# Kernel tuning notes

Measured on AMD Instinct MI355X. Metric: run time of the kernel, lower is better.

The kernel has to match this reference:

```python
import jax, jax.numpy as jnp
import numpy as np

N, DIM = 1024, 3
DEPTH, H1, H2, NF = 4, 64, 32, 8
L = 1.0
PI = np.pi


def _h2_features(x):
    n, dim = x.shape
    rij = x[:, None, :] - x[None, :, :]                       # (n, n, dim)
    eye = jnp.eye(n, dtype=x.dtype)
    # distance of periodic sine displacement, diagonal regularized then zeroed
    r = jnp.linalg.norm(jnp.sin(PI * rij / L) + eye[..., None], axis=-1) * (1.0 - eye)
    kf = jnp.arange(1, NF + 1, dtype=x.dtype)                 # (NF,)
    ang = (2.0 * PI / L) * rij[:, :, None, :] * kf[:, None]   # (n, n, NF, dim)
    # original concat order per frequency k: cos block (dim cols) then sin block
    cs = jnp.stack([jnp.cos(ang), jnp.sin(ang)], axis=3)      # (n, n, NF, 2, dim)
    return jnp.concatenate([r[..., None], cs.reshape(n, n, 2 * NF * dim)], axis=-1)


def _h1_init(t, n):
    t = jnp.reshape(t, ())
    kf = jnp.arange(1, NF + 1, dtype=jnp.float32)
    ang = 2.0 * PI * t * kf                                   # (NF,)
    feats = jnp.concatenate([t[None], jnp.stack([jnp.cos(ang), jnp.sin(ang)], axis=1).reshape(-1)])
    return jnp.broadcast_to(feats[None, :], (n, 1 + 2 * NF))  # (n, 17)


def _combine(h1, h2):
    n = h1.shape[0]
    g2 = jnp.mean(h2, axis=0)                                 # (n, h2f)
    g1 = jnp.broadcast_to(jnp.mean(h1, axis=0, keepdims=True), h1.shape)
    return jnp.concatenate([h1, g1, g2], axis=1)


def _forward(x, t, W1, b1, W2, b2, Wf):
    n, dim = x.shape
    h1 = _h1_init(t, n)
    h2 = _h2_features(x)
    for d in range(DEPTH - 1):
        f = _combine(h1, h2)
        h1u = jnp.tanh(f @ W1[d] + b1[d])
        h2u = jnp.tanh(h2 @ W2[d] + b2[d])
        h1 = h1u + h1 if d > 0 else h1u
        h2 = h2u + h2 if d > 0 else h2u
    f = _combine(h1, h2)
    h1 = jnp.tanh(f @ W1[-1] + b1[-1]) + h1
    force = jnp.clip(2.0 * x, -10.0, 10.0)
    return -(h1 @ Wf) * force


def setup_inputs():
    key = jax.random.key(0)
    ks = jax.random.split(key, 20)
    s = 0.01
    inp = {
        "x": jax.random.normal(ks[0], (N, DIM), jnp.float32),
        "t": jax.random.uniform(ks[1], (), dtype=jnp.float32),
    }
    f0 = 2 * (1 + 2 * NF) + (1 + 2 * NF * DIM)  # 83
    fl = 2 * H1 + H2                            # 160
    w1_in = [f0, fl, fl, fl]
    w2_in = [1 + 2 * NF * DIM, H2, H2]
    for d in range(DEPTH):
        inp[f"W1_{d}"] = s * jax.random.normal(ks[2 + d], (w1_in[d], H1), jnp.float32)
        inp[f"b1_{d}"] = jnp.zeros((H1,), jnp.float32)
    for d in range(DEPTH - 1):
        inp[f"W2_{d}"] = s * jax.random.normal(ks[8 + d], (w2_in[d], H2), jnp.float32)
        inp[f"b2_{d}"] = jnp.zeros((H2,), jnp.float32)
    inp["Wf"] = s * jax.random.normal(ks[15], (H1, DIM), jnp.float32)
    return inp


def reference(x, t, W1_0, b1_0, W1_1, b1_1, W1_2, b1_2, W1_3, b1_3,
              W2_0, b2_0, W2_1, b2_1, W2_2, b2_2, Wf):
    W1 = [W1_0, W1_1, W1_2, W1_3]
    b1 = [b1_0, b1_1, b1_2, b1_3]
    W2 = [W2_0, W2_1, W2_2]
    b2 = [b2_0, b2_1, b2_2]
    return _forward(x, t, W1, b1, W2, b2, Wf)
```

## Files before the change

### kernel.cpp

```cpp
#include <hip/hip_runtime.h>
#include <math.h>


#define NP 1024

static const size_t OF_TROW = 0;
static const size_t OF_CSUM = OF_TROW + NP*56;
static const size_t OF_SSUM = OF_CSUM + 24;
static const size_t OF_HSUM = OF_SSUM + 24;
static const size_t OF_CNT  = OF_HSUM + 192;
static const size_t OF_RACC = OF_CNT + 4;
static const size_t OF_M0   = OF_RACC + NP;
static const size_t OF_M1   = OF_M0 + NP*32;
static const size_t OF_M2   = OF_M1 + NP*32;

__device__ __forceinline__ float ftanh(float x) {
    float e = __expf(2.0f * x);
    return 1.0f - __fdividef(2.0f, e + 1.0f);
}

__global__ __launch_bounds__(1024) void k1_tables(
    const float* __restrict__ X,
    float* __restrict__ TROW,
    float* __restrict__ CSUM, float* __restrict__ SSUM,
    float* __restrict__ HSUM, int* __restrict__ CNT)
{
    const int i = threadIdx.x;
    float ck[24], sk[24], cp[3], sp[3];
#pragma unroll
    for (int d = 0; d < 3; ++d) {
        float x = X[i*3 + d];
        sincospif(x, &sp[d], &cp[d]);
#pragma unroll
        for (int k = 0; k < 8; ++k) {
            float s, c;
            sincospif(2.0f*(float)(k+1)*x, &s, &c);
            ck[k*3 + d] = c;  sk[k*3 + d] = s;
        }
    }
    float4* row = (float4*)(TROW + (size_t)i*56);
#pragma unroll
    for (int t = 0; t < 12; ++t)
        row[t] = make_float4(ck[2*t], sk[2*t], ck[2*t+1], sk[2*t+1]);
    row[12] = make_float4(cp[0], sp[0], cp[1], sp[1]);
    row[13] = make_float4(cp[2], sp[2], 0.f, 0.f);

    __shared__ float part[48*16];
    const int lane = i & 63, wv = i >> 6;
#pragma unroll
    for (int v = 0; v < 24; ++v) {
        float a = ck[v], b = sk[v];
#pragma unroll
        for (int off = 32; off; off >>= 1) {
            a += __shfl_down(a, off, 64);
            b += __shfl_down(b, off, 64);
        }
        if (lane == 0) { part[v*16 + wv] = a; part[(24+v)*16 + wv] = b; }
    }
    __syncthreads();
    if (i < 48) {
        float s = 0.f;
#pragma unroll
        for (int w = 0; w < 16; ++w) s += part[i*16 + w];
        if (i < 24) CSUM[i] = s; else SSUM[i-24] = s;
    }
    if (i < 192) HSUM[i] = 0.0f;
    if (i == 200) CNT[0] = 0;
}

__global__ __launch_bounds__(512, 4) void k2_pairs(
    const float* __restrict__ W20, const float* __restrict__ b20,
    const float* __restrict__ W21, const float* __restrict__ b21,
    const float* __restrict__ W22, const float* __restrict__ b22,
    const float* __restrict__ TROW,
    float* __restrict__ RACC, float* __restrict__ M0,
    float* __restrict__ M1, float* __restrict__ M2)
{
    __shared__ __align__(16) float sH0[128*32];
    __shared__ __align__(16) float sH1[128*32];
    __shared__ __align__(16) float sJ[56];
    __shared__ __align__(16) float sPQ[24*64];

    const int tid  = threadIdx.x;
    const int lane = tid & 63;
    const int wid  = __builtin_amdgcn_readfirstlane(tid >> 6);
    const int c0   = wid * 4;
    const int j    = blockIdx.x;
    const int lx   = lane & 7;

    if (tid < 14) ((float4*)sJ)[tid] = ((const float4*)(TROW + (size_t)j*56))[tid];

    const float b0x = b20[c0+0], b0y = b20[c0+1], b0z = b20[c0+2], b0w = b20[c0+3];
    const float b1x = b21[c0+0], b1y = b21[c0+1], b1z = b21[c0+2], b1w = b21[c0+3];
    const float b2x = b22[c0+0], b2y = b22[c0+1], b2z = b22[c0+2], b2w = b22[c0+3];
    __syncthreads();

    for (int idx = tid; idx < 24*64; idx += 512) {
        const int kd = idx >> 6;
        const int e  = idx & 63;
        const int c  = e & 31;
        const int k = kd/3, d = kd - k*3;
        const float wcv = W20[(1 + k*6 + d)*32 + c];
        const float wsv = W20[(4 + k*6 + d)*32 + c];
        const float cj = sJ[2*kd], sj = sJ[2*kd+1];
        sPQ[idx] = (e < 32) ? fmaf(cj, wcv, -(sj*wsv))
                            : fmaf(sj, wcv,   cj*wsv);
    }
    __syncthreads();

    float4* H0a = (float4*)sH0 + lane*8;
    float4* H0b = (float4*)sH0 + (lane+64)*8;
    float4* H1a = (float4*)sH1 + lane*8;
    float4* H1b = (float4*)sH1 + (lane+64)*8;

    float a0x=0.f,a0y=0.f,a0z=0.f,a0w=0.f;
    float a1x=0.f,a1y=0.f,a1z=0.f,a1w=0.f;
    float a2x=0.f,a2y=0.f,a2z=0.f,a2w=0.f;
    float racc = 0.f;

#pragma unroll 1
    for (int tile = 0; tile < 8; ++tile) {
        const float4* rowA = (const float4*)(TROW + (size_t)(tile*128 + lane)*56);
        const float4* rowB = rowA + 14*64;

        float rA, rB;
        {
            const float4 pa = rowA[12], pb = rowA[13];
            float s0 = fmaf(pa.y, sJ[48], -(pa.x * sJ[49]));
            float s1 = fmaf(pa.w, sJ[50], -(pa.z * sJ[51]));
            float s2 = fmaf(pb.y, sJ[52], -(pb.x * sJ[53]));
            rA = sqrtf(fmaf(s0, s0, fmaf(s1, s1, s2*s2)));
        }
        {
            const float4 pa = rowB[12], pb = rowB[13];
            float s0 = fmaf(pa.y, sJ[48], -(pa.x * sJ[49]));
            float s1 = fmaf(pa.w, sJ[50], -(pa.z * sJ[51]));
            float s2 = fmaf(pb.y, sJ[52], -(pb.x * sJ[53]));
            rB = sqrtf(fmaf(s0, s0, fmaf(s1, s1, s2*s2)));
        }
        racc += rA + rB;

        float zA0, zA1, zA2, zA3, zB0, zB1, zB2, zB3;
        {
            const float* w = W20 + c0;
            zA0 = fmaf(rA, w[0], b0x); zA1 = fmaf(rA, w[1], b0y);
            zA2 = fmaf(rA, w[2], b0z); zA3 = fmaf(rA, w[3], b0w);
            zB0 = fmaf(rB, w[0], b0x); zB1 = fmaf(rB, w[1], b0y);
            zB2 = fmaf(rB, w[2], b0z); zB3 = fmaf(rB, w[3], b0w);
        }
#pragma unroll
        for (int t = 0; t < 12; ++t) {
            const float4 fA = rowA[t], fB = rowB[t];
#pragma unroll
            for (int sub = 0; sub < 2; ++sub) {
                const int kd = 2*t + sub;
                const float4 P = *(const float4*)(sPQ + kd*64 + c0);
                const float4 Q = *(const float4*)(sPQ + kd*64 + 32 + c0);
                const float ciA = sub ? fA.z : fA.x, siA = sub ? fA.w : fA.y;
                const float ciB = sub ? fB.z : fB.x, siB = sub ? fB.w : fB.y;
                zA0 = fmaf(ciA, P.x, fmaf(siA, Q.x, zA0));
                zA1 = fmaf(ciA, P.y, fmaf(siA, Q.y, zA1));
                zA2 = fmaf(ciA, P.z, fmaf(siA, Q.z, zA2));
                zA3 = fmaf(ciA, P.w, fmaf(siA, Q.w, zA3));
                zB0 = fmaf(ciB, P.x, fmaf(siB, Q.x, zB0));
                zB1 = fmaf(ciB, P.y, fmaf(siB, Q.y, zB1));
                zB2 = fmaf(ciB, P.z, fmaf(siB, Q.z, zB2));
                zB3 = fmaf(ciB, P.w, fmaf(siB, Q.w, zB3));
            }
        }

        float hA0 = ftanh(zA0), hA1 = ftanh(zA1), hA2 = ftanh(zA2), hA3 = ftanh(zA3);
        float hB0 = ftanh(zB0), hB1 = ftanh(zB1), hB2 = ftanh(zB2), hB3 = ftanh(zB3);
        a0x += hA0 + hB0; a0y += hA1 + hB1; a0z += hA2 + hB2; a0w += hA3 + hB3;
        H0a[wid ^ lx] = make_float4(hA0, hA1, hA2, hA3);
        H0b[wid ^ lx] = make_float4(hB0, hB1, hB2, hB3);
        __syncthreads();

        zA0 = b1x; zA1 = b1y; zA2 = b1z; zA3 = b1w;
        zB0 = b1x; zB1 = b1y; zB2 = b1z; zB3 = b1w;
#pragma unroll
        for (int kc = 0; kc < 8; ++kc) {
            const float4 hA = H0a[kc ^ lx];
            const float4 hB = H0b[kc ^ lx];
            const float* w0 = W21 + (kc*4+0)*32 + c0;
            const float* w1 = W21 + (kc*4+1)*32 + c0;
            const float* w2 = W21 + (kc*4+2)*32 + c0;
            const float* w3 = W21 + (kc*4+3)*32 + c0;
            zA0 = fmaf(hA.x,w0[0], fmaf(hA.y,w1[0], fmaf(hA.z,w2[0], fmaf(hA.w,w3[0], zA0))));
            zA1 = fmaf(hA.x,w0[1], fmaf(hA.y,w1[1], fmaf(hA.z,w2[1], fmaf(hA.w,w3[1], zA1))));
            zA2 = fmaf(hA.x,w0[2], fmaf(hA.y,w1[2], fmaf(hA.z,w2[2], fmaf(hA.w,w3[2], zA2))));
            zA3 = fmaf(hA.x,w0[3], fmaf(hA.y,w1[3], fmaf(hA.z,w2[3], fmaf(hA.w,w3[3], zA3))));
            zB0 = fmaf(hB.x,w0[0], fmaf(hB.y,w1[0], fmaf(hB.z,w2[0], fmaf(hB.w,w3[0], zB0))));
            zB1 = fmaf(hB.x,w0[1], fmaf(hB.y,w1[1], fmaf(hB.z,w2[1], fmaf(hB.w,w3[1], zB1))));
            zB2 = fmaf(hB.x,w0[2], fmaf(hB.y,w1[2], fmaf(hB.z,w2[2], fmaf(hB.w,w3[2], zB2))));
            zB3 = fmaf(hB.x,w0[3], fmaf(hB.y,w1[3], fmaf(hB.z,w2[3], fmaf(hB.w,w3[3], zB3))));
        }
        hA0 = ftanh(zA0) + hA0; hA1 = ftanh(zA1) + hA1;
        hA2 = ftanh(zA2) + hA2; hA3 = ftanh(zA3) + hA3;
        hB0 = ftanh(zB0) + hB0; hB1 = ftanh(zB1) + hB1;
        hB2 = ftanh(zB2) + hB2; hB3 = ftanh(zB3) + hB3;
        a1x += hA0 + hB0; a1y += hA1 + hB1; a1z += hA2 + hB2; a1w += hA3 + hB3;
        H1a[wid ^ lx] = make_float4(hA0, hA1, hA2, hA3);
        H1b[wid ^ lx] = make_float4(hB0, hB1, hB2, hB3);
        __syncthreads();

        zA0 = b2x; zA1 = b2y; zA2 = b2z; zA3 = b2w;
        zB0 = b2x; zB1 = b2y; zB2 = b2z; zB3 = b2w;
#pragma unroll
        for (int kc = 0; kc < 8; ++kc) {
            const float4 hA = H1a[kc ^ lx];
            const float4 hB = H1b[kc ^ lx];
            const float* w0 = W22 + (kc*4+0)*32 + c0;
            const float* w1 = W22 + (kc*4+1)*32 + c0;
            const float* w2 = W22 + (kc*4+2)*32 + c0;
            const float* w3 = W22 + (kc*4+3)*32 + c0;
            zA0 = fmaf(hA.x,w0[0], fmaf(hA.y,w1[0], fmaf(hA.z,w2[0], fmaf(hA.w,w3[0], zA0))));
            zA1 = fmaf(hA.x,w0[1], fmaf(hA.y,w1[1], fmaf(hA.z,w2[1], fmaf(hA.w,w3[1], zA1))));
            zA2 = fmaf(hA.x,w0[2], fmaf(hA.y,w1[2], fmaf(hA.z,w2[2], fmaf(hA.w,w3[2], zA2))));
            zA3 = fmaf(hA.x,w0[3], fmaf(hA.y,w1[3], fmaf(hA.z,w2[3], fmaf(hA.w,w3[3], zA3))));
            zB0 = fmaf(hB.x,w0[0], fmaf(hB.y,w1[0], fmaf(hB.z,w2[0], fmaf(hB.w,w3[0], zB0))));
            zB1 = fmaf(hB.x,w0[1], fmaf(hB.y,w1[1], fmaf(hB.z,w2[1], fmaf(hB.w,w3[1], zB1))));
            zB2 = fmaf(hB.x,w0[2], fmaf(hB.y,w1[2], fmaf(hB.z,w2[2], fmaf(hB.w,w3[2], zB2))));
            zB3 = fmaf(hB.x,w0[3], fmaf(hB.y,w1[3], fmaf(hB.z,w2[3], fmaf(hB.w,w3[3], zB3))));
        }
        a2x += ftanh(zA0) + hA0 + ftanh(zB0) + hB0;
        a2y += ftanh(zA1) + hA1 + ftanh(zB1) + hB1;
        a2z += ftanh(zA2) + hA2 + ftanh(zB2) + hB2;
        a2w += ftanh(zA3) + hA3 + ftanh(zB3) + hB3;
    }

#pragma unroll
    for (int mask = 1; mask < 64; mask <<= 1) {
        a0x += __shfl_xor(a0x, mask, 64); a0y += __shfl_xor(a0y, mask, 64);
        a0z += __shfl_xor(a0z, mask, 64); a0w += __shfl_xor(a0w, mask, 64);
        a1x += __shfl_xor(a1x, mask, 64); a1y += __shfl_xor(a1y, mask, 64);
        a1z += __shfl_xor(a1z, mask, 64); a1w += __shfl_xor(a1w, mask, 64);
        a2x += __shfl_xor(a2x, mask, 64); a2y += __shfl_xor(a2y, mask, 64);
        a2z += __shfl_xor(a2z, mask, 64); a2w += __shfl_xor(a2w, mask, 64);
        racc += __shfl_xor(racc, mask, 64);
    }
    if (lane == 0) {
        *(float4*)(M0 + j*32 + c0) = make_float4(a0x, a0y, a0z, a0w);
        *(float4*)(M1 + j*32 + c0) = make_float4(a1x, a1y, a1z, a1w);
        *(float4*)(M2 + j*32 + c0) = make_float4(a2x, a2y, a2z, a2w);
        if (wid == 0) RACC[j] = racc;
    }
}

#define FMA8(fv, wptr) do { \
    const float4* w4_ = (const float4*)(wptr); \
    float4 a_ = w4_[0], b_ = w4_[1]; \
    z[0]=fmaf((fv),a_.x,z[0]); z[1]=fmaf((fv),a_.y,z[1]); \
    z[2]=fmaf((fv),a_.z,z[2]); z[3]=fmaf((fv),a_.w,z[3]); \
    z[4]=fmaf((fv),b_.x,z[4]); z[5]=fmaf((fv),b_.y,z[5]); \
    z[6]=fmaf((fv),b_.z,z[6]); z[7]=fmaf((fv),b_.w,z[7]); \
} while (0)

#define HSTR 65

__device__ __forceinline__ void hsum_atomic(float* HS, const float h[8],
                                            int tid, int c0) {
    float hs[8];
#pragma unroll
    for (int u = 0; u < 8; ++u) {
        hs[u] = h[u];
#pragma unroll
        for (int mask = 8; mask < 64; mask <<= 1)
            hs[u] += __shfl_xor(hs[u], mask, 64);
    }
    if (((tid & 63) >> 3) == 0) {
#pragma unroll
        for (int u = 0; u < 8; ++u) atomicAdd(&HS[c0 + u], hs[u]);
    }
}

__device__ __forceinline__ void gsync(int* cnt, int target, int tid) {
    __syncthreads();
    if (tid == 0) {
        __threadfence();
        atomicAdd(cnt, 1);
        while (atomicAdd(cnt, 0) < target) {}
    }
    __syncthreads();
}

__global__ __launch_bounds__(128) void h1_all(
    const float* __restrict__ Tsc,
    const float* __restrict__ W10, const float* __restrict__ b10,
    const float* __restrict__ W11, const float* __restrict__ b11,
    const float* __restrict__ W12, const float* __restrict__ b12,
    const float* __restrict__ W13, const float* __restrict__ b13,
    const float* __restrict__ Wf,  const float* __restrict__ X,
    const float* __restrict__ TROW,
    const float* __restrict__ CSUM, const float* __restrict__ SSUM,
    const float* __restrict__ RACC,
    const float* __restrict__ M0, const float* __restrict__ M1,
    const float* __restrict__ M2,
    float* __restrict__ HSUM, int* __restrict__ CNT,
    float* __restrict__ out)
{
    __shared__ float sH[16*HSTR];
    __shared__ float sG[64];
    const int tid = threadIdx.x;
    const int gid = blockIdx.x*128 + tid;
    const int j = gid >> 3, qq = gid & 7, c0 = qq*8;
    const int lj = tid >> 3;
    const float inv_n = 1.0f/1024.0f;
    float* myrow = sH + lj*HSTR;

    float h[8];
    {
        const float t = Tsc[0];
        float z[8];
#pragma unroll
        for (int u = 0; u < 8; ++u) z[u] = b10[c0+u];
        FMA8(t, W10 + 0*64 + c0);
        FMA8(t, W10 + 17*64 + c0);
#pragma unroll
        for (int k = 0; k < 8; ++k) {
            float s, c; sincospif(2.0f*(float)(k+1)*t, &s, &c);
            FMA8(c, W10 + (1+2*k)*64 + c0);
            FMA8(c, W10 + (18+2*k)*64 + c0);
            FMA8(s, W10 + (2+2*k)*64 + c0);
            FMA8(s, W10 + (19+2*k)*64 + c0);
        }
        FMA8(RACC[j]*inv_n, W10 + 34*64 + c0);
        const float4* rj = (const float4*)(TROW + (size_t)j*56);
#pragma unroll
        for (int tt = 0; tt < 12; ++tt) {
            float4 v = rj[tt];
#pragma unroll
            for (int sub = 0; sub < 2; ++sub) {
                const int kd = 2*tt + sub;
                float cj = sub ? v.z : v.x;
                float sj = sub ? v.w : v.y;
                float Cb = CSUM[kd]*inv_n, Sb = SSUM[kd]*inv_n;
                float cm = fmaf(cj, Cb, sj*Sb);
                float sm = fmaf(Sb, cj, -(Cb*sj));
                int k = kd/3, d = kd - k*3;
                FMA8(cm, W10 + (35 + k*6 + d)*64 + c0);
                FMA8(sm, W10 + (38 + k*6 + d)*64 + c0);
            }
        }
#pragma unroll
        for (int u = 0; u < 8; ++u) {
            h[u] = ftanh(z[u]);
            myrow[c0+u] = h[u];
        }
        hsum_atomic(HSUM + 0*64, h, tid, c0);
    }
    gsync(CNT, 64, tid);
    if (tid < 64) sG[tid] = __hip_atomic_load(&HSUM[0*64+tid], __ATOMIC_RELAXED,
                                              __HIP_MEMORY_SCOPE_AGENT) * inv_n;
    __syncthreads();

#pragma unroll 1
    for (int L = 1; L <= 2; ++L) {
        const float* W = (L == 1) ? W11 : W12;
        const float* b = (L == 1) ? b11 : b12;
        const float* M = (L == 1) ? M0  : M1;
        float z[8];
#pragma unroll
        for (int u = 0; u < 8; ++u) z[u] = b[c0+u];
#pragma unroll 4
        for (int p = 0; p < 64; ++p) FMA8(myrow[p], W + p*64 + c0);
#pragma unroll 4
        for (int p = 0; p < 64; ++p) FMA8(sG[p], W + (64+p)*64 + c0);
        const float* mrow = M + j*32;
#pragma unroll 4
        for (int p = 0; p < 32; ++p) FMA8(mrow[p]*inv_n, W + (128+p)*64 + c0);
#pragma unroll
        for (int u = 0; u < 8; ++u) h[u] = ftanh(z[u]) + myrow[c0+u];
        __syncthreads();
#pragma unroll
        for (int u = 0; u < 8; ++u) myrow[c0+u] = h[u];
        hsum_atomic(HSUM + L*64, h, tid, c0);
        gsync(CNT, 64*(L+1), tid);
        if (tid < 64) sG[tid] = __hip_atomic_load(&HSUM[L*64+tid], __ATOMIC_RELAXED,
                                                  __HIP_MEMORY_SCOPE_AGENT) * inv_n;
        __syncthreads();
    }

    {
        float z[8];
#pragma unroll
        for (int u = 0; u < 8; ++u) z[u] = b13[c0+u];
#pragma unroll 4
        for (int p = 0; p < 64; ++p) FMA8(myrow[p], W13 + p*64 + c0);
#pragma unroll 4
        for (int p = 0; p < 64; ++p) FMA8(sG[p], W13 + (64+p)*64 + c0);
        const float* mrow = M2 + j*32;
#pragma unroll 4
        for (int p = 0; p < 32; ++p) FMA8(mrow[p]*inv_n, W13 + (128+p)*64 + c0);
#pragma unroll
        for (int u = 0; u < 8; ++u) h[u] = ftanh(z[u]) + myrow[c0+u];

        float p0 = 0.f, p1 = 0.f, p2 = 0.f;
#pragma unroll
        for (int u = 0; u < 8; ++u) {
            const float* wf = Wf + (c0+u)*3;
            p0 = fmaf(h[u], wf[0], p0);
            p1 = fmaf(h[u], wf[1], p1);
            p2 = fmaf(h[u], wf[2], p2);
        }
#pragma unroll
        for (int m = 1; m < 8; m <<= 1) {
            p0 += __shfl_xor(p0, m, 64);
            p1 += __shfl_xor(p1, m, 64);
            p2 += __shfl_xor(p2, m, 64);
        }
        if (qq == 0) {
#pragma unroll
            for (int d = 0; d < 3; ++d) {
                float fx = 2.0f * X[j*3 + d];
                fx = fminf(fmaxf(fx, -10.0f), 10.0f);
                float s = (d == 0 ? p0 : (d == 1 ? p1 : p2));
                out[j*3 + d] = -s * fx;
            }
        }
    }
}

extern "C" void kernel_launch(void* const* d_in, const int* in_sizes, int n_in,
                              void* d_out, int out_size, void* d_ws, size_t ws_size,
                              hipStream_t stream)
{
    const float* X   = (const float*)d_in[0];
    const float* Tsc = (const float*)d_in[1];
    const float* W10 = (const float*)d_in[2];  const float* b10 = (const float*)d_in[3];
    const float* W11 = (const float*)d_in[4];  const float* b11 = (const float*)d_in[5];
    const float* W12 = (const float*)d_in[6];  const float* b12 = (const float*)d_in[7];
    const float* W13 = (const float*)d_in[8];  const float* b13 = (const float*)d_in[9];
    const float* W20 = (const float*)d_in[10]; const float* b20 = (const float*)d_in[11];
    const float* W21 = (const float*)d_in[12]; const float* b21 = (const float*)d_in[13];
    const float* W22 = (const float*)d_in[14]; const float* b22 = (const float*)d_in[15];
    const float* Wf  = (const float*)d_in[16];

    float* ws  = (float*)d_ws;
    float* out = (float*)d_out;

    float* TROW = ws + OF_TROW;
    float* CSUM = ws + OF_CSUM; float* SSUM = ws + OF_SSUM;
    float* HSUM = ws + OF_HSUM; int*   CNT  = (int*)(ws + OF_CNT);
    float* RACC = ws + OF_RACC;
    float* M0 = ws + OF_M0; float* M1 = ws + OF_M1; float* M2 = ws + OF_M2;

    k1_tables<<<1, 1024, 0, stream>>>(X, TROW, CSUM, SSUM, HSUM, CNT);
    k2_pairs<<<NP, 512, 0, stream>>>(W20, b20, W21, b21, W22, b22,
                                     TROW, RACC, M0, M1, M2);
    h1_all<<<64, 128, 0, stream>>>(Tsc, W10, b10, W11, b11, W12, b12, W13, b13,
                                   Wf, X, TROW, CSUM, SSUM, RACC,
                                   M0, M1, M2, HSUM, CNT, out);
}
```

Before: 414.7 us.

## Use packed float2 FMA in pair MLP and regrid h1 kernel to 8 blocks

The pair-MLP inner loops in k2_pairs now hold the A and B row accumulators as float2 vectors and use elementwise FMA, so the compiler can emit packed FP32 FMA instructions. The h1_all kernel is relaunched as 8 blocks of 1024 threads instead of 64 blocks of 128, which cuts the number of blocks taking part in each grid-wide barrier. The barrier spin loop now uses an acquire load with s_sleep instead of repeated atomicAdd polling. Larger blocks raise shared memory and register pressure per block and use fewer CUs for h1_all, and the packed form depends on the compiler keeping operands paired without extra moves.

Result: slower. 515.0 us (+24.2%).

```diff
diff --git a/kernel.cpp b/kernel.cpp
--- a/kernel.cpp
+++ b/kernel.cpp
@@ -3,6 +3,12 @@
 
 
 #define NP 1024
+
+typedef float f2 __attribute__((ext_vector_type(2)));
+static __device__ __forceinline__ f2 splat2(float s) { f2 v; v.x = s; v.y = s; return v; }
+static __device__ __forceinline__ f2 fma2(f2 a, f2 b, f2 c) {
+    return __builtin_elementwise_fma(a, b, c);
+}
 
 static const size_t OF_TROW = 0;
 static const size_t OF_CSUM = OF_TROW + NP*56;
@@ -140,13 +146,14 @@
         }
         racc += rA + rB;
 
-        float zA0, zA1, zA2, zA3, zB0, zB1, zB2, zB3;
+        f2 z0, z1, z2, z3;
         {
             const float* w = W20 + c0;
-            zA0 = fmaf(rA, w[0], b0x); zA1 = fmaf(rA, w[1], b0y);
-            zA2 = fmaf(rA, w[2], b0z); zA3 = fmaf(rA, w[3], b0w);
-            zB0 = fmaf(rB, w[0], b0x); zB1 = fmaf(rB, w[1], b0y);
-            zB2 = fmaf(rB, w[2], b0z); zB3 = fmaf(rB, w[3], b0w);
+            f2 rv; rv.x = rA; rv.y = rB;
+            z0 = fma2(rv, splat2(w[0]), splat2(b0x));
+            z1 = fma2(rv, splat2(w[1]), splat2(b0y));
+            z2 = fma2(rv, splat2(w[2]), splat2(b0z));
+            z3 = fma2(rv, splat2(w[3]), splat2(b0w));
         }
 #pragma unroll
         for (int t = 0; t < 12; ++t) {
@@ -156,28 +163,24 @@
                 const int kd = 2*t + sub;
                 const float4 P = *(const float4*)(sPQ + kd*64 + c0);
                 const float4 Q = *(const float4*)(sPQ + kd*64 + 32 + c0);
-                const float ciA = sub ? fA.z : fA.x, siA = sub ? fA.w : fA.y;
-                const float ciB = sub ? fB.z : fB.x, siB = sub ? fB.w : fB.y;
-                zA0 = fmaf(ciA, P.x, fmaf(siA, Q.x, zA0));
-                zA1 = fmaf(ciA, P.y, fmaf(siA, Q.y, zA1));
-                zA2 = fmaf(ciA, P.z, fmaf(siA, Q.z, zA2));
-                zA3 = fmaf(ciA, P.w, fmaf(siA, Q.w, zA3));
-                zB0 = fmaf(ciB, P.x, fmaf(siB, Q.x, zB0));
-                zB1 = fmaf(ciB, P.y, fmaf(siB, Q.y, zB1));
-                zB2 = fmaf(ciB, P.z, fmaf(siB, Q.z, zB2));
-                zB3 = fmaf(ciB, P.w, fmaf(siB, Q.w, zB3));
+                f2 ci, si;
+                ci.x = sub ? fA.z : fA.x;  ci.y = sub ? fB.z : fB.x;
+                si.x = sub ? fA.w : fA.y;  si.y = sub ? fB.w : fB.y;
+                z0 = fma2(ci, splat2(P.x), fma2(si, splat2(Q.x), z0));
+                z1 = fma2(ci, splat2(P.y), fma2(si, splat2(Q.y), z1));
+                z2 = fma2(ci, splat2(P.z), fma2(si, splat2(Q.z), z2));
+                z3 = fma2(ci, splat2(P.w), fma2(si, splat2(Q.w), z3));
             }
         }
 
-        float hA0 = ftanh(zA0), hA1 = ftanh(zA1), hA2 = ftanh(zA2), hA3 = ftanh(zA3);
-        float hB0 = ftanh(zB0), hB1 = ftanh(zB1), hB2 = ftanh(zB2), hB3 = ftanh(zB3);
+        float hA0 = ftanh(z0.x), hA1 = ftanh(z1.x), hA2 = ftanh(z2.x), hA3 = ftanh(z3.x);
+        float hB0 = ftanh(z0.y), hB1 = ftanh(z1.y), hB2 = ftanh(z2.y), hB3 = ftanh(z3.y);
         a0x += hA0 + hB0; a0y += hA1 + hB1; a0z += hA2 + hB2; a0w += hA3 + hB3;
         H0a[wid ^ lx] = make_float4(hA0, hA1, hA2, hA3);
         H0b[wid ^ lx] = make_float4(hB0, hB1, hB2, hB3);
         __syncthreads();
 
-        zA0 = b1x; zA1 = b1y; zA2 = b1z; zA3 = b1w;
-        zB0 = b1x; zB1 = b1y; zB2 = b1z; zB3 = b1w;
+        z0 = splat2(b1x); z1 = splat2(b1y); z2 = splat2(b1z); z3 = splat2(b1w);
 #pragma unroll
         for (int kc = 0; kc < 8; ++kc) {
             const float4 hA = H0a[kc ^ lx];
@@ -186,26 +189,28 @@
             const float* w1 = W21 + (kc*4+1)*32 + c0;
             const float* w2 = W21 + (kc*4+2)*32 + c0;
             const float* w3 = W21 + (kc*4+3)*32 + c0;
-            zA0 = fmaf(hA.x,w0[0], fmaf(hA.y,w1[0], fmaf(hA.z,w2[0], fmaf(hA.w,w3[0], zA0))));
-            zA1 = fmaf(hA.x,w0[1], fmaf(hA.y,w1[1], fmaf(hA.z,w2[1], fmaf(hA.w,w3[1], zA1))));
-            zA2 = fmaf(hA.x,w0[2], fmaf(hA.y,w1[2], fmaf(hA.z,w2[2], fmaf(hA.w,w3[2], zA2))));
-            zA3 = fmaf(hA.x,w0[3], fmaf(hA.y,w1[3], fmaf(hA.z,w2[3], fmaf(hA.w,w3[3], zA3))));
-            zB0 = fmaf(hB.x,w0[0], fmaf(hB.y,w1[0], fmaf(hB.z,w2[0], fmaf(hB.w,w3[0], zB0))));
-            zB1 = fmaf(hB.x,w0[1], fmaf(hB.y,w1[1], fmaf(hB.z,w2[1], fmaf(hB.w,w3[1], zB1))));
-            zB2 = fmaf(hB.x,w0[2], fmaf(hB.y,w1[2], fmaf(hB.z,w2[2], fmaf(hB.w,w3[2], zB2))));
-            zB3 = fmaf(hB.x,w0[3], fmaf(hB.y,w1[3], fmaf(hB.z,w2[3], fmaf(hB.w,w3[3], zB3))));
-        }
-        hA0 = ftanh(zA0) + hA0; hA1 = ftanh(zA1) + hA1;
-        hA2 = ftanh(zA2) + hA2; hA3 = ftanh(zA3) + hA3;
-        hB0 = ftanh(zB0) + hB0; hB1 = ftanh(zB1) + hB1;
-        hB2 = ftanh(zB2) + hB2; hB3 = ftanh(zB3) + hB3;
+            f2 hx, hy, hz, hw;
+            hx.x = hA.x; hx.y = hB.x;  hy.x = hA.y; hy.y = hB.y;
+            hz.x = hA.z; hz.y = hB.z;  hw.x = hA.w; hw.y = hB.w;
+            z0 = fma2(hx, splat2(w0[0]), fma2(hy, splat2(w1[0]),
+                 fma2(hz, splat2(w2[0]), fma2(hw, splat2(w3[0]), z0))));
+            z1 = fma2(hx, splat2(w0[1]), fma2(hy, splat2(w1[1]),
+                 fma2(hz, splat2(w2[1]), fma2(hw, splat2(w3[1]), z1))));
+            z2 = fma2(hx, splat2(w0[2]), fma2(hy, splat2(w1[2]),
+                 fma2(hz, splat2(w2[2]), fma2(hw, splat2(w3[2]), z2))));
+            z3 = fma2(hx, splat2(w0[3]), fma2(hy, splat2(w1[3]),
+                 fma2(hz, splat2(w2[3]), fma2(hw, splat2(w3[3]), z3))));
+        }
+        hA0 = ftanh(z0.x) + hA0; hA1 = ftanh(z1.x) + hA1;
+        hA2 = ftanh(z2.x) + hA2; hA3 = ftanh(z3.x) + hA3;
+        hB0 = ftanh(z0.y) + hB0; hB1 = ftanh(z1.y) + hB1;
+        hB2 = ftanh(z2.y) + hB2; hB3 = ftanh(z3.y) + hB3;
         a1x += hA0 + hB0; a1y += hA1 + hB1; a1z += hA2 + hB2; a1w += hA3 + hB3;
         H1a[wid ^ lx] = make_float4(hA0, hA1, hA2, hA3);
         H1b[wid ^ lx] = make_float4(hB0, hB1, hB2, hB3);
         __syncthreads();
 
-        zA0 = b2x; zA1 = b2y; zA2 = b2z; zA3 = b2w;
-        zB0 = b2x; zB1 = b2y; zB2 = b2z; zB3 = b2w;
+        z0 = splat2(b2x); z1 = splat2(b2y); z2 = splat2(b2z); z3 = splat2(b2w);
 #pragma unroll
         for (int kc = 0; kc < 8; ++kc) {
             const float4 hA = H1a[kc ^ lx];
@@ -214,19 +219,22 @@
             const float* w1 = W22 + (kc*4+1)*32 + c0;
             const float* w2 = W22 + (kc*4+2)*32 + c0;
             const float* w3 = W22 + (kc*4+3)*32 + c0;
-            zA0 = fmaf(hA.x,w0[0], fmaf(hA.y,w1[0], fmaf(hA.z,w2[0], fmaf(hA.w,w3[0], zA0))));
-            zA1 = fmaf(hA.x,w0[1], fmaf(hA.y,w1[1], fmaf(hA.z,w2[1], fmaf(hA.w,w3[1], zA1))));
-            zA2 = fmaf(hA.x,w0[2], fmaf(hA.y,w1[2], fmaf(hA.z,w2[2], fmaf(hA.w,w3[2], zA2))));
-            zA3 = fmaf(hA.x,w0[3], fmaf(hA.y,w1[3], fmaf(hA.z,w2[3], fmaf(hA.w,w3[3], zA3))));
-            zB0 = fmaf(hB.x,w0[0], fmaf(hB.y,w1[0], fmaf(hB.z,w2[0], fmaf(hB.w,w3[0], zB0))));
-            zB1 = fmaf(hB.x,w0[1], fmaf(hB.y,w1[1], fmaf(hB.z,w2[1], fmaf(hB.w,w3[1], zB1))));
-            zB2 = fmaf(hB.x,w0[2], fmaf(hB.y,w1[2], fmaf(hB.z,w2[2], fmaf(hB.w,w3[2], zB2))));
-            zB3 = fmaf(hB.x,w0[3], fmaf(hB.y,w1[3], fmaf(hB.z,w2[3], fmaf(hB.w,w3[3], zB3))));
-        }
-        a2x += ftanh(zA0) + hA0 + ftanh(zB0) + hB0;
-        a2y += ftanh(zA1) + hA1 + ftanh(zB1) + hB1;
-        a2z += ftanh(zA2) + hA2 + ftanh(zB2) + hB2;
-        a2w += ftanh(zA3) + hA3 + ftanh(zB3) + hB3;
+            f2 hx, hy, hz, hw;
+            hx.x = hA.x; hx.y = hB.x;  hy.x = hA.y; hy.y = hB.y;
+            hz.x = hA.z; hz.y = hB.z;  hw.x = hA.w; hw.y = hB.w;
+            z0 = fma2(hx, splat2(w0[0]), fma2(hy, splat2(w1[0]),
+                 fma2(hz, splat2(w2[0]), fma2(hw, splat2(w3[0]), z0))));
+            z1 = fma2(hx, splat2(w0[1]), fma2(hy, splat2(w1[1]),
+                 fma2(hz, splat2(w2[1]), fma2(hw, splat2(w3[1]), z1))));
+            z2 = fma2(hx, splat2(w0[2]), fma2(hy, splat2(w1[2]),
+                 fma2(hz, splat2(w2[2]), fma2(hw, splat2(w3[2]), z2))));
+            z3 = fma2(hx, splat2(w0[3]), fma2(hy, splat2(w1[3]),
+                 fma2(hz, splat2(w2[3]), fma2(hw, splat2(w3[3]), z3))));
+        }
+        a2x += ftanh(z0.x) + hA0 + ftanh(z0.y) + hB0;
+        a2y += ftanh(z1.x) + hA1 + ftanh(z1.y) + hB1;
+        a2z += ftanh(z2.x) + hA2 + ftanh(z2.y) + hB2;
+        a2w += ftanh(z3.x) + hA3 + ftanh(z3.y) + hB3;
     }
 
 #pragma unroll
@@ -279,12 +287,14 @@
     if (tid == 0) {
         __threadfence();
         atomicAdd(cnt, 1);
-        while (atomicAdd(cnt, 0) < target) {}
-    }
-    __syncthreads();
-}
-
-__global__ __launch_bounds__(128) void h1_all(
+        while (__hip_atomic_load(cnt, __ATOMIC_ACQUIRE,
+                                 __HIP_MEMORY_SCOPE_AGENT) < target)
+            __builtin_amdgcn_s_sleep(8);
+    }
+    __syncthreads();
+}
+
+__global__ __launch_bounds__(1024) void h1_all(
     const float* __restrict__ Tsc,
     const float* __restrict__ W10, const float* __restrict__ b10,
     const float* __restrict__ W11, const float* __restrict__ b11,
@@ -299,10 +309,10 @@
     float* __restrict__ HSUM, int* __restrict__ CNT,
     float* __restrict__ out)
 {
-    __shared__ float sH[16*HSTR];
+    __shared__ float sH[128*HSTR];
     __shared__ float sG[64];
     const int tid = threadIdx.x;
-    const int gid = blockIdx.x*128 + tid;
+    const int gid = blockIdx.x*1024 + tid;
     const int j = gid >> 3, qq = gid & 7, c0 = qq*8;
     const int lj = tid >> 3;
     const float inv_n = 1.0f/1024.0f;
@@ -349,7 +359,7 @@
         }
         hsum_atomic(HSUM + 0*64, h, tid, c0);
     }
-    gsync(CNT, 64, tid);
+    gsync(CNT, 8, tid);
     if (tid < 64) sG[tid] = __hip_atomic_load(&HSUM[0*64+tid], __ATOMIC_RELAXED,
                                               __HIP_MEMORY_SCOPE_AGENT) * inv_n;
     __syncthreads();
@@ -375,7 +385,7 @@
 #pragma unroll
         for (int u = 0; u < 8; ++u) myrow[c0+u] = h[u];
         hsum_atomic(HSUM + L*64, h, tid, c0);
-        gsync(CNT, 64*(L+1), tid);
+        gsync(CNT, 8*(L+1), tid);
         if (tid < 64) sG[tid] = __hip_atomic_load(&HSUM[L*64+tid], __ATOMIC_RELAXED,
                                                   __HIP_MEMORY_SCOPE_AGENT) * inv_n;
         __syncthreads();
@@ -448,7 +458,7 @@
     k1_tables<<<1, 1024, 0, stream>>>(X, TROW, CSUM, SSUM, HSUM, CNT);
     k2_pairs<<<NP, 512, 0, stream>>>(W20, b20, W21, b21, W22, b22,
                                      TROW, RACC, M0, M1, M2);
-    h1_all<<<64, 128, 0, stream>>>(Tsc, W10, b10, W11, b11, W12, b12, W13, b13,
+    h1_all<<<8, 1024, 0, stream>>>(Tsc, W10, b10, W11, b11, W12, b12, W13, b13,
                                    Wf, X, TROW, CSUM, SSUM, RACC,
                                    M0, M1, M2, HSUM, CNT, out);
 }
```
